# Performance work log

Hardware: AMD Instinct MI355X
Metric: run time of the kernel (lower is better)

Reference implementation:

```python
import jax, jax.numpy as jnp
import numpy as np

BETA = 1e-8
ALPHA = 0.5
CHOOSE_K = 128
MEMORY_SIZE = 65536
KEY_DIM = 256
BATCH = 1024


def _l2norm(x, axis=-1, eps=1e-12):
    return x / jnp.sqrt(jnp.sum(x * x, axis=axis, keepdims=True) + eps)


def setup_inputs() -> dict:
    key = jax.random.key(0)
    k1, k2, k3 = jax.random.split(key, 3)
    q = _l2norm(jax.random.normal(k1, (BATCH, KEY_DIM), dtype=jnp.float32))
    memory_key = _l2norm(jax.random.normal(k2, (MEMORY_SIZE, KEY_DIM), dtype=jnp.float32))
    # module init: hist[:] = 1e-5; add small random variation so topk is non-degenerate
    memory_hist = 1e-5 + 1e-3 * jax.random.uniform(k3, (MEMORY_SIZE,), dtype=jnp.float32)
    # module init: values = ones, second half zeroed
    memory_values = jnp.concatenate([
        jnp.ones((MEMORY_SIZE // 2,), dtype=jnp.float32),
        jnp.zeros((MEMORY_SIZE - MEMORY_SIZE // 2,), dtype=jnp.float32),
    ])
    return {"q": q, "memory_key": memory_key,
            "memory_hist": memory_hist, "memory_values": memory_values}


def reference(q, memory_key, memory_hist, memory_values):
    # obtain_topk over FULL memory: dense similarity [B, M]
    sims = jnp.matmul(q, memory_key.T)                      # [B, M]
    scores = jnp.exp(sims - 1.0) * (memory_hist + BETA)[None, :]
    _, k_idxs = jax.lax.top_k(scores, CHOOSE_K)             # [B, K]

    # gather reduced memory at topk indices
    red_keys = memory_key[k_idxs]                           # [B, K, D]
    red_hist = memory_hist[k_idxs] * ALPHA                  # [B, K]
    red_vals = memory_values[k_idxs]                        # [B, K]

    # posterior over the K gathered slots
    sim_k = jnp.einsum('bd,bkd->bk', q, red_keys)           # [B, K]
    joint = jnp.exp(sim_k - 1.0) * (red_hist + BETA)        # [B, K]
    posterior = joint / jnp.sum(joint, axis=1, keepdims=True)
    result = jnp.sum(posterior * red_vals, axis=1)          # [B]
    return result
```

## Files before the change

kernel.cpp:

```cpp
#include <hip/hip_runtime.h>

#define BATCH   1024
#define MSIZE   65536
#define KDIM    256
#define CHOOSEK 128
#define SELK    160
#define T0  156.0f
#define T1  160.0f
#define T2  164.0f
#define BETA    1e-8f
#define ALPHA   0.5f
#define KSC  425.0f
#define KOFF 7.2f
#define LVLW ((size_t)1024 * 1024)

typedef short bf16x8 __attribute__((ext_vector_type(8)));
typedef float f32x4  __attribute__((ext_vector_type(4)));

__device__ inline unsigned int pack2bf(float a, float b) {
    unsigned int ua = __float_as_uint(a);
    unsigned int ub = __float_as_uint(b);
    ua += 0x7fffu + ((ua >> 16) & 1u);
    ub += 0x7fffu + ((ub >> 16) & 1u);
    return (ua >> 16) | (ub & 0xffff0000u);
}

__global__ __launch_bounds__(256)
void convert_kernel(const float* __restrict__ q, const float* __restrict__ key,
                    const float* __restrict__ hist,
                    unsigned short* __restrict__ qs, unsigned short* __restrict__ kbf,
                    float* __restrict__ Ltab)
{
    const int bid = blockIdx.x, tid = threadIdx.x;
    if (bid < 8192) {
        const int t = bid * 256 + tid;
        const int l = t & 63, f = t >> 6;
        const int i = f & 3, ks = (f >> 2) & 7, wnh = (f >> 5) & 1, nt = f >> 6;
        const int row = nt * 128 + wnh * 64 + i * 16 + (l & 15);
        const int col = ks * 32 + (l >> 4) * 8;
        const float* src = key + (size_t)row * KDIM + col;
        float4 a = *(const float4*)src, b = *(const float4*)(src + 4);
        ((uint4*)kbf)[t] = make_uint4(pack2bf(a.x, a.y), pack2bf(a.z, a.w),
                                      pack2bf(b.x, b.y), pack2bf(b.z, b.w));
    } else if (bid < 8320) {
        const int f = (bid - 8192) * 256 + tid;
        const int l = f & 63, j = (f >> 6) & 3, ks = (f >> 8) & 7;
        const int wmg = (f >> 11) & 1, bt = f >> 12;
        const int r = bt * 128 + wmg * 64 + j * 16 + (l & 15);
        const int c = ks * 32 + (l >> 4) * 8;
        const float* src = q + (size_t)r * KDIM + c;
        float4 a = *(const float4*)src, b = *(const float4*)(src + 4);
        ((uint4*)qs)[f] = make_uint4(pack2bf(a.x, a.y), pack2bf(a.z, a.w),
                                     pack2bf(b.x, b.y), pack2bf(b.z, b.w));
    } else {
        const int n = (bid - 8320) * 256 + tid;
        Ltab[n] = (logf(hist[n] + BETA) + KOFF) * KSC;
    }
}

__global__ __launch_bounds__(256)
void score_kernel(const unsigned short* __restrict__ qs,
                  const unsigned short* __restrict__ kbf,
                  const float* __restrict__ Ltab,
                  unsigned long long* __restrict__ gmask)
{
    const int tid = threadIdx.x;
    const int bid = blockIdx.x;
    const int bt = (bid >> 3) & 7;
    const int b0 = bt * 128;
    const int nt = (bid & 7) | ((bid >> 6) << 3);
    const int n0 = nt * 128;
    const int lane = tid & 63, wave = tid >> 6;
    const int wm = (wave >> 1) * 64, wn = (wave & 1) * 64;
    const int l15 = lane & 15, l4 = lane >> 4;

    f32x4 acc[4][4] = {};

    const bf16x8* qw = (const bf16x8*)qs  + (size_t)((bt * 2 + (wave >> 1)) * 32) * 64 + lane;
    const bf16x8* kw = (const bf16x8*)kbf + (size_t)((nt * 2 + (wave &  1)) * 32) * 64 + lane;

    bf16x8 qf[2][4], kf[2][4];
#pragma unroll
    for (int j = 0; j < 4; ++j) { qf[0][j] = qw[j * 64]; kf[0][j] = kw[j * 64]; }

#pragma unroll
    for (int s = 0; s < 8; ++s) {
        const int cur = s & 1;
        if (s < 7) {
#pragma unroll
            for (int j = 0; j < 4; ++j) {
                qf[cur ^ 1][j] = qw[((s + 1) * 4 + j) * 64];
                kf[cur ^ 1][j] = kw[((s + 1) * 4 + j) * 64];
            }
        }
        __builtin_amdgcn_s_setprio(1);
#pragma unroll
        for (int i = 0; i < 4; ++i)
#pragma unroll
            for (int j = 0; j < 4; ++j)
                acc[i][j] = __builtin_amdgcn_mfma_f32_16x16x32_bf16(kf[cur][i], qf[cur][j], acc[i][j], 0, 0, 0);
        __builtin_amdgcn_s_setprio(0);
    }

    float4 Lv[4];
#pragma unroll
    for (int i = 0; i < 4; ++i)
        Lv[i] = *(const float4*)&Ltab[n0 + wn + i * 16 + l4 * 4];
#pragma unroll
    for (int j = 0; j < 4; ++j) {
        const int rb = b0 + wm + j * 16 + l15;
        unsigned int lo0 = 0, hi0 = 0, lo1 = 0, hi1 = 0, lo2 = 0, hi2 = 0;
#pragma unroll
        for (int i = 0; i < 4; ++i) {
            const float* lv = (const float*)&Lv[i];
            unsigned int n0b = 0, n1b = 0, n2b = 0;
#pragma unroll
            for (int reg = 0; reg < 4; ++reg) {
                float x = fmaf(acc[i][j][reg], KSC, lv[reg]);
                n0b |= (x >= T0 ? 1u : 0u) << reg;
                n1b |= (x >= T1 ? 1u : 0u) << reg;
                n2b |= (x >= T2 ? 1u : 0u) << reg;
            }
            const int sh = (i & 1) * 16 + l4 * 4;
            if (i < 2) { lo0 |= n0b << sh; lo1 |= n1b << sh; lo2 |= n2b << sh; }
            else       { hi0 |= n0b << sh; hi1 |= n1b << sh; hi2 |= n2b << sh; }
        }
        lo0 |= __shfl_xor(lo0, 16, 64); hi0 |= __shfl_xor(hi0, 16, 64);
        lo0 |= __shfl_xor(lo0, 32, 64); hi0 |= __shfl_xor(hi0, 32, 64);
        lo1 |= __shfl_xor(lo1, 16, 64); hi1 |= __shfl_xor(hi1, 16, 64);
        lo1 |= __shfl_xor(lo1, 32, 64); hi1 |= __shfl_xor(hi1, 32, 64);
        lo2 |= __shfl_xor(lo2, 16, 64); hi2 |= __shfl_xor(hi2, 16, 64);
        lo2 |= __shfl_xor(lo2, 32, 64); hi2 |= __shfl_xor(hi2, 32, 64);
        if (l4 == 0) {
            const size_t ofs = ((size_t)(nt * 2) + (wn >> 6)) * 1024 + rb;
            gmask[ofs]            = ((unsigned long long)hi0 << 32) | lo0;
            gmask[ofs + LVLW]     = ((unsigned long long)hi1 << 32) | lo1;
            gmask[ofs + 2 * LVLW] = ((unsigned long long)hi2 << 32) | lo2;
        }
    }
}

__global__ __launch_bounds__(256, 4)
void select_kernel(const float* __restrict__ q,
                   const float* __restrict__ key,
                   const float* __restrict__ hist,
                   const float* __restrict__ vals,
                   const unsigned long long* __restrict__ gmask,
                   float* __restrict__ out)
{
    const int b   = blockIdx.x;
    const int tid = threadIdx.x;

    __shared__ __align__(16) float qs[KDIM];
    __shared__ int   scal[2];
    __shared__ int   cidx[1024];
    __shared__ float csc[1024], cjj[1024], cjv[1024];
    __shared__ float wred[8];

    qs[tid] = q[(size_t)b * KDIM + tid];
    if (tid < 2) scal[tid] = 0;
    __syncthreads();

    unsigned long long mw[4];
    int myc = 0;
    int lvlsel = 2;
    for (;;) {
        myc = 0;
#pragma unroll
        for (int k = 0; k < 4; ++k) {
            mw[k] = gmask[(size_t)lvlsel * LVLW + (size_t)(tid + k * 256) * 1024 + b];
            myc += __popcll(mw[k]);
        }
        { int ws = myc;
#pragma unroll
          for (int off = 32; off > 0; off >>= 1) ws += __shfl_xor(ws, off, 64);
          if ((tid & 63) == 0) atomicAdd((unsigned int*)&scal[0], (unsigned int)ws); }
        __syncthreads();
        const int c = scal[0];
        __syncthreads();
        if ((c >= SELK && c <= 1024) || lvlsel == 0) break;
        if (tid == 0) scal[0] = 0;
        __syncthreads();
        --lvlsel;
    }

    int base = atomicAdd(&scal[1], myc);
#pragma unroll
    for (int k = 0; k < 4; ++k) {
        unsigned long long m = mw[k];
        while (m) {
            int bpos = __builtin_ctzll(m);
            m &= m - 1;
            if (base < 1024) cidx[base] = (tid + k * 256) * 64 + bpos;
            ++base;
        }
    }
    __syncthreads();
    const int ncand = min(scal[1], 1024);

    const int gid = tid >> 4, gll = tid & 15;
    const float4* q4 = (const float4*)qs;
    for (int i = gid; i < ncand; i += 16) {
        const int idx = cidx[i];
        const float4* kp = (const float4*)(key + (size_t)idx * KDIM);
        float p = 0.f;
#pragma unroll
        for (int u = 0; u < 4; ++u) {
            float4 kk = kp[gll * 4 + u];
            float4 qq = q4[gll * 4 + u];
            p += kk.x * qq.x + kk.y * qq.y + kk.z * qq.z + kk.w * qq.w;
        }
#pragma unroll
        for (int off = 1; off < 16; off <<= 1) p += __shfl_xor(p, off, 64);
        if (gll == 0) {
            float e = expf(p - 1.0f);
            float h = hist[idx];
            csc[i] = e * (h + BETA);
            float j = e * (ALPHA * h + BETA);
            cjj[i] = j;
            cjv[i] = j * vals[idx];
        }
    }
    __syncthreads();

    const int wave = tid >> 6, lane = tid & 63;
    float pn = 0.f, pd = 0.f;
    for (int i = tid; i < ncand; i += 256) {
        float si = csc[i]; int ii = cidx[i]; int rank = 0;
        for (int t = 0; t < ncand; ++t) {
            float st = csc[t];
            rank += (st > si || (st == si && cidx[t] < ii)) ? 1 : 0;
        }
        if (rank < CHOOSEK) { pn += cjv[i]; pd += cjj[i]; }
    }
#pragma unroll
    for (int off = 32; off > 0; off >>= 1) {
        pn += __shfl_xor(pn, off, 64);
        pd += __shfl_xor(pd, off, 64);
    }
    if (lane == 0) { wred[wave] = pn; wred[4 + wave] = pd; }
    __syncthreads();
    if (tid == 0) {
        float n = wred[0] + wred[1] + wred[2] + wred[3];
        float d = wred[4] + wred[5] + wred[6] + wred[7];
        out[b] = n / d;
    }
}

extern "C" void kernel_launch(void* const* d_in, const int* in_sizes, int n_in,
                              void* d_out, int out_size, void* d_ws, size_t ws_size,
                              hipStream_t stream)
{
    (void)in_sizes; (void)n_in; (void)out_size; (void)ws_size;
    const float* q    = (const float*)d_in[0];
    const float* key  = (const float*)d_in[1];
    const float* hist = (const float*)d_in[2];
    const float* vals = (const float*)d_in[3];
    float* out = (float*)d_out;

    unsigned short* kbf= (unsigned short*)d_ws;
    unsigned short* qsw= (unsigned short*)((char*)d_ws + ((size_t)32 << 20));
    float*          Lt = (float*)((char*)d_ws + ((size_t)32 << 20) + (512 << 10));
    unsigned long long* gmask = (unsigned long long*)((char*)d_ws + ((size_t)33 << 20));

    convert_kernel<<<8576, 256, 0, stream>>>(q, key, hist, qsw, kbf, Lt);
    score_kernel<<<4096, 256, 0, stream>>>(qsw, kbf, Lt, gmask);
    select_kernel<<<BATCH, 256, 0, stream>>>(q, key, hist, vals, gmask, out);
}
```

Measured before the change: 193.7 us.

## Write per-lane 16-bit threshold masks and decode permuted bit layout in select

The score kernel no longer merges threshold bits across the four lane groups with twelve cross-lane shuffles followed by a single-lane 64-bit store. Each lane now stores its own 16-bit mask per level, so the 64-bit word ends up in a permuted bit order. The select kernel undoes that permutation when it converts bit positions to candidate indices. Select blocks are also remapped to a strided batch order, presumably to spread key-gather locality, at the cost of narrower scattered 2-byte global stores.

```diff
diff --git a/kernel.cpp b/kernel.cpp
--- a/kernel.cpp
+++ b/kernel.cpp
@@ -62,7 +62,7 @@
 void score_kernel(const unsigned short* __restrict__ qs,
                   const unsigned short* __restrict__ kbf,
                   const float* __restrict__ Ltab,
-                  unsigned long long* __restrict__ gmask)
+                  unsigned short* __restrict__ gm16)
 {
     const int tid = threadIdx.x;
     const int bid = blockIdx.x;
@@ -73,6 +73,7 @@
     const int lane = tid & 63, wave = tid >> 6;
     const int wm = (wave >> 1) * 64, wn = (wave & 1) * 64;
     const int l15 = lane & 15, l4 = lane >> 4;
+    const int widx = nt * 2 + (wave & 1);
 
     f32x4 acc[4][4] = {};
 
@@ -109,34 +110,22 @@
 #pragma unroll
     for (int j = 0; j < 4; ++j) {
         const int rb = b0 + wm + j * 16 + l15;
-        unsigned int lo0 = 0, hi0 = 0, lo1 = 0, hi1 = 0, lo2 = 0, hi2 = 0;
+        unsigned int p0 = 0, p1 = 0, p2 = 0;
 #pragma unroll
         for (int i = 0; i < 4; ++i) {
             const float* lv = (const float*)&Lv[i];
-            unsigned int n0b = 0, n1b = 0, n2b = 0;
 #pragma unroll
             for (int reg = 0; reg < 4; ++reg) {
                 float x = fmaf(acc[i][j][reg], KSC, lv[reg]);
-                n0b |= (x >= T0 ? 1u : 0u) << reg;
-                n1b |= (x >= T1 ? 1u : 0u) << reg;
-                n2b |= (x >= T2 ? 1u : 0u) << reg;
+                p0 |= (x >= T0 ? 1u : 0u) << (i * 4 + reg);
+                p1 |= (x >= T1 ? 1u : 0u) << (i * 4 + reg);
+                p2 |= (x >= T2 ? 1u : 0u) << (i * 4 + reg);
             }
-            const int sh = (i & 1) * 16 + l4 * 4;
-            if (i < 2) { lo0 |= n0b << sh; lo1 |= n1b << sh; lo2 |= n2b << sh; }
-            else       { hi0 |= n0b << sh; hi1 |= n1b << sh; hi2 |= n2b << sh; }
-        }
-        lo0 |= __shfl_xor(lo0, 16, 64); hi0 |= __shfl_xor(hi0, 16, 64);
-        lo0 |= __shfl_xor(lo0, 32, 64); hi0 |= __shfl_xor(hi0, 32, 64);
-        lo1 |= __shfl_xor(lo1, 16, 64); hi1 |= __shfl_xor(hi1, 16, 64);
-        lo1 |= __shfl_xor(lo1, 32, 64); hi1 |= __shfl_xor(hi1, 32, 64);
-        lo2 |= __shfl_xor(lo2, 16, 64); hi2 |= __shfl_xor(hi2, 16, 64);
-        lo2 |= __shfl_xor(lo2, 32, 64); hi2 |= __shfl_xor(hi2, 32, 64);
-        if (l4 == 0) {
-            const size_t ofs = ((size_t)(nt * 2) + (wn >> 6)) * 1024 + rb;
-            gmask[ofs]            = ((unsigned long long)hi0 << 32) | lo0;
-            gmask[ofs + LVLW]     = ((unsigned long long)hi1 << 32) | lo1;
-            gmask[ofs + 2 * LVLW] = ((unsigned long long)hi2 << 32) | lo2;
-        }
+        }
+        const size_t u16i = ((size_t)widx * 1024 + rb) * 4 + l4;
+        gm16[u16i]                = (unsigned short)p0;
+        gm16[u16i + LVLW * 4]     = (unsigned short)p1;
+        gm16[u16i + 2 * LVLW * 4] = (unsigned short)p2;
     }
 }
 
@@ -148,7 +137,8 @@
                    const unsigned long long* __restrict__ gmask,
                    float* __restrict__ out)
 {
-    const int b   = blockIdx.x;
+    const int bid = blockIdx.x;
+    const int b   = ((bid & 7) << 7) | (bid >> 3);
     const int tid = threadIdx.x;
 
     __shared__ __align__(16) float qs[KDIM];
@@ -189,9 +179,10 @@
     for (int k = 0; k < 4; ++k) {
         unsigned long long m = mw[k];
         while (m) {
-            int bpos = __builtin_ctzll(m);
+            int p = __builtin_ctzll(m);
             m &= m - 1;
-            if (base < 1024) cidx[base] = (tid + k * 256) * 64 + bpos;
+            int col = ((p >> 2) & 3) * 16 + ((p >> 4) << 2) + (p & 3);
+            if (base < 1024) cidx[base] = (tid + k * 256) * 64 + col;
             ++base;
         }
     }
@@ -264,6 +255,6 @@
     unsigned long long* gmask = (unsigned long long*)((char*)d_ws + ((size_t)33 << 20));
 
     convert_kernel<<<8576, 256, 0, stream>>>(q, key, hist, qsw, kbf, Lt);
-    score_kernel<<<4096, 256, 0, stream>>>(qsw, kbf, Lt, gmask);
+    score_kernel<<<4096, 256, 0, stream>>>(qsw, kbf, Lt, (unsigned short*)gmask);
     select_kernel<<<BATCH, 256, 0, stream>>>(q, key, hist, vals, gmask, out);
 }
```

Result: faster. 182.8 us (-5.6%).
